# Optimization experiments

Measured on AMD Instinct MI355X. Metric: run time of the kernel, lower is better.

Reference implementation:

```python
import jax, jax.numpy as jnp
import numpy as np

ITERS_MAX = 10
CORR_THRESHOLD = 0.5


def setup_inputs() -> dict:
    key = jax.random.key(0)
    k1, k2, k3 = jax.random.split(key, 3)
    B, M, N = 8, 2048, 2048
    pc_src = jax.random.normal(k1, (B, 3, M), dtype=jnp.float32)
    # dest = src plus small perturbation so NN correspondences within threshold exist
    pc_dest = pc_src + 0.05 * jax.random.normal(k2, (B, 3, N), dtype=jnp.float32)
    init_R = jnp.broadcast_to(jnp.eye(3, dtype=jnp.float32), (B, 3, 3))
    init_t = 0.01 * jax.random.normal(k3, (B, 3, 1), dtype=jnp.float32)
    return {"pc_src": pc_src, "pc_dest": pc_dest, "init_R": init_R, "init_t": init_t}


def _icp(pc_src, pc_dest, init_R, init_t):
    # valid dest points: not exactly the zero vector (matches torch mask logic)
    valid = jnp.sum(pc_dest != 0.0, axis=1) == 3          # (B, N)
    any_valid = jnp.any(valid, axis=1)                    # (B,)
    src = pc_src[0].T                                     # (M, 3) -- original uses batch-0 source only
    dest = jnp.transpose(pc_dest, (0, 2, 1))              # (B, N, 3)
    dest_sq = jnp.sum(dest * dest, axis=-1)               # (B, N)
    thr2 = CORR_THRESHOLD * CORR_THRESHOLD

    def corr(Rc, tc):
        # transformed source points: (B, M, 3)
        p = jnp.einsum('bij,mj->bmi', Rc, src) + jnp.transpose(tc, (0, 2, 1))
        # all-pairs squared distances (B, M, N) -- the compute-heavy NN search
        d2 = (jnp.sum(p * p, axis=-1)[:, :, None] + dest_sq[:, None, :]
              - 2.0 * jnp.einsum('bmi,bni->bmn', p, dest))
        d2 = jnp.where(valid[:, None, :], d2, jnp.inf)
        idx = jnp.argmin(d2, axis=-1)                     # (B, M)
        q = jnp.take_along_axis(dest, idx[..., None], axis=1)   # (B, M, 3)
        # recompute exact squared residual from p, q (stable + differentiable)
        d2min = jnp.maximum(jnp.sum((p - q) ** 2, axis=-1), 0.0)  # (B, M)
        w = ((d2min < thr2) & any_valid[:, None]).astype(p.dtype)  # inlier weights
        return q, w, d2min

    def step(carry, _):
        Rc, tc = carry
        q, w, _ = corr(Rc, tc)
        wsum = jnp.sum(w, axis=-1)                        # (B,)
        safe = jnp.maximum(wsum, 1.0)
        mu_p = jnp.einsum('bm,mi->bi', w, src) / safe[:, None]
        mu_q = jnp.einsum('bm,bmi->bi', w, q) / safe[:, None]
        Pc = src[None, :, :] - mu_p[:, None, :]           # (B, M, 3)
        Qc = q - mu_q[:, None, :]                         # (B, M, 3)
        # Kabsch / Umeyama (no scaling): H = sum_m w p_c q_c^T
        H = jnp.einsum('bm,bmi,bmj->bij', w, Pc, Qc)
        U, S, Vt = jnp.linalg.svd(H)
        V = jnp.transpose(Vt, (0, 2, 1))
        d = jnp.linalg.det(V) * jnp.linalg.det(U)         # reflection fix
        D = jnp.stack([jnp.ones_like(d), jnp.ones_like(d), d], axis=-1)
        Rn = jnp.einsum('bij,bj,bkj->bik', V, D, U)       # V diag(1,1,d) U^T
        tn = (mu_q - jnp.einsum('bij,bj->bi', Rn, mu_p))[:, :, None]
        ok = (wsum > 0.0)[:, None, None]
        Rn = jnp.where(ok, Rn, Rc)
        tn = jnp.where(ok, tn, tc)
        return (Rn, tn), None

    (Rf, tf), _ = jax.lax.scan(step, (init_R, init_t), None, length=ITERS_MAX)

    # inlier RMSE at the final transform (Open3D icp_sol.inlier_rmse analogue)
    _, w, d2 = corr(Rf, tf)
    wsum = jnp.sum(w, axis=-1, keepdims=True)             # (B, 1)
    rmse = jnp.sqrt(jnp.sum(w * d2, axis=-1, keepdims=True) / jnp.maximum(wsum, 1.0))
    mse = jnp.where(wsum > 0.0, rmse, jnp.nan)            # (B, 1); nan if no valid dest
    return Rf, tf, mse


def reference(pc_src, pc_dest, init_R, init_t):
    return _icp(pc_src, pc_dest, init_R, init_t)
```

## Files before the change

### kernel.cpp

```cpp
#include <hip/hip_runtime.h>
#include <math.h>

#define BB 8
#define MM 2048
#define NNP 2048
#define THR2 0.25f
#define NITER 10
#define NPART 17
#define TPB 1024
#define WPB 16
#define BPB 32
#define GRIDB (BB * BPB)
#define TM 8
#define HALF (NNP / 2)
#define STEPS (HALF / 64)

__global__ void pack_kernel(const float* __restrict__ pc_dest,
                            float4* __restrict__ destp,
                            float* __restrict__ anyvalid)
{
    const int b = blockIdx.x;
    const int tid = threadIdx.x;
    __shared__ int anyf;
    if (tid == 0) anyf = 0;
    __syncthreads();
    int local = 0;
    for (int n = tid; n < NNP; n += blockDim.x) {
        const float dx = pc_dest[(b * 3 + 0) * NNP + n];
        const float dy = pc_dest[(b * 3 + 1) * NNP + n];
        const float dz = pc_dest[(b * 3 + 2) * NNP + n];
        const int valid = (dx != 0.0f) && (dy != 0.0f) && (dz != 0.0f);
        const float dd = dx * dx + dy * dy + dz * dz;
        destp[b * NNP + n] = make_float4(dx, dy, dz, valid ? dd : INFINITY);
        local |= valid;
    }
    if (local) atomicOr(&anyf, 1);
    __syncthreads();
    if (tid == 0) anyvalid[b] = (anyf != 0) ? 1.0f : 0.0f;
}

__device__ void kabsch3f(const float H[3][3], float R[3][3])
{
    float A[3][3];
    for (int i = 0; i < 3; ++i)
        for (int j = 0; j < 3; ++j) {
            float s = 0.0f;
            for (int k = 0; k < 3; ++k) s += H[k][i] * H[k][j];
            A[i][j] = s;
        }
    float V[3][3] = {{1,0,0},{0,1,0},{0,0,1}};
    const float nrm = A[0][0]*A[0][0] + A[1][1]*A[1][1] + A[2][2]*A[2][2] + 1e-30f;
    for (int sweep = 0; sweep < 8; ++sweep) {
        const float off = A[0][1]*A[0][1] + A[0][2]*A[0][2] + A[1][2]*A[1][2];
        if (off < 1e-14f * nrm) break;
        for (int pi = 0; pi < 3; ++pi) {
            const int p = (pi == 2) ? 1 : 0;
            const int q = (pi == 0) ? 1 : 2;
            const float apq = A[p][q];
            if (apq == 0.0f) continue;
            const float theta = (A[q][q] - A[p][p]) / (2.0f * apq);
            const float t = ((theta >= 0.0f) ? 1.0f : -1.0f) / (fabsf(theta) + sqrtf(theta * theta + 1.0f));
            const float c = 1.0f / sqrtf(t * t + 1.0f);
            const float s = t * c;
            const float app = A[p][p], aqq = A[q][q];
            A[p][p] = app - t * apq;
            A[q][q] = aqq + t * apq;
            A[p][q] = 0.0f; A[q][p] = 0.0f;
            const int r = 3 - p - q;
            const float arp = A[r][p], arq = A[r][q];
            A[r][p] = c * arp - s * arq; A[p][r] = A[r][p];
            A[r][q] = s * arp + c * arq; A[q][r] = A[r][q];
            for (int rr = 0; rr < 3; ++rr) {
                const float vrp = V[rr][p], vrq = V[rr][q];
                V[rr][p] = c * vrp - s * vrq;
                V[rr][q] = s * vrp + c * vrq;
            }
        }
    }
    float lam[3] = {A[0][0], A[1][1], A[2][2]};
    int ord[3] = {0, 1, 2};
    for (int i = 0; i < 2; ++i)
        for (int j = i + 1; j < 3; ++j)
            if (lam[ord[j]] > lam[ord[i]]) { const int tmp = ord[i]; ord[i] = ord[j]; ord[j] = tmp; }
    float Vs[3][3], U[3][3];
    for (int k = 0; k < 3; ++k) {
        const int c0 = ord[k];
        const float sk = sqrtf(fmaxf(lam[c0], 0.0f));
        const float inv = (sk > 1e-12f) ? 1.0f / sk : 0.0f;
        for (int i = 0; i < 3; ++i) {
            Vs[i][k] = V[i][c0];
            U[i][k] = (H[i][0] * V[0][c0] + H[i][1] * V[1][c0] + H[i][2] * V[2][c0]) * inv;
        }
    }
    const float detH = H[0][0] * (H[1][1] * H[2][2] - H[1][2] * H[2][1])
                     - H[0][1] * (H[1][0] * H[2][2] - H[1][2] * H[2][0])
                     + H[0][2] * (H[1][0] * H[2][1] - H[1][1] * H[2][0]);
    const float d = (detH < 0.0f) ? -1.0f : 1.0f;
    for (int i = 0; i < 3; ++i)
        for (int j = 0; j < 3; ++j)
            R[i][j] = Vs[i][0] * U[j][0] + Vs[i][1] * U[j][1] + d * Vs[i][2] * U[j][2];
}

__global__ __launch_bounds__(TPB, 4) void corr_kernel(
    const int it,
    const float* __restrict__ pc_src,
    const float4* __restrict__ destp,
    const float* __restrict__ anyvalid,
    const float* __restrict__ init_R,
    const float* __restrict__ init_t,
    float* __restrict__ partials,
    float* __restrict__ out)
{
    const int blk = blockIdx.x;
    const int b = blk / BPB;
    const int cblk = blk % BPB;
    const int tid = threadIdx.x;
    const int wid = tid >> 6;
    const int lane = tid & 63;
    const int pairid = wid >> 1;
    const int half = wid & 1;

    __shared__ float4 ds[NNP];
    __shared__ float sred[BPB * NPART];
    __shared__ float sminV[WPB][TM];
    __shared__ int   sminI[WPB][TM];
    __shared__ float smom[WPB / 2][NPART];
    __shared__ float Sfin[NPART];
    __shared__ float Rt[12];

    const float4* db = destp + b * NNP;
    ds[tid]       = db[tid];
    ds[tid + TPB] = db[tid + TPB];

    if (it > 0) {
        if (tid < BPB * NPART) {
            const int row = tid / NPART, k = tid % NPART;
            sred[tid] = partials[(size_t)(((it - 1) * BB + b) * BPB + row) * 32 + k];
        }
    } else {
        if (tid < 9) Rt[tid] = init_R[b * 9 + tid];
        if (tid < 3) Rt[9 + tid] = init_t[b * 3 + tid];
    }
    __syncthreads();

    if (it > 0) {
        if (tid < NPART) {
            float s = 0.0f;
            #pragma unroll
            for (int c = 0; c < BPB; ++c) s += sred[c * NPART + tid];
            Sfin[tid] = s;
        }
        __syncthreads();
        if (tid == 0) {
            const float wsum = Sfin[0];
            if (wsum >= 0.5f) {
                const float safe = fmaxf(wsum, 1.0f);
                const float inv = 1.0f / safe;
                float mup[3], muq[3];
                for (int i = 0; i < 3; ++i) { mup[i] = Sfin[1 + i] * inv; muq[i] = Sfin[4 + i] * inv; }
                float H[3][3];
                for (int i = 0; i < 3; ++i)
                    for (int j = 0; j < 3; ++j)
                        H[i][j] = (Sfin[7 + i * 3 + j] * inv) - mup[i] * muq[j];
                float R[3][3];
                kabsch3f(H, R);
                for (int i = 0; i < 3; ++i) {
                    for (int j = 0; j < 3; ++j) Rt[i * 3 + j] = R[i][j];
                    Rt[9 + i] = muq[i] - (R[i][0] * mup[0] + R[i][1] * mup[1] + R[i][2] * mup[2]);
                }
            } else {
                for (int k = 0; k < 9; ++k) Rt[k] = init_R[b * 9 + k];
                for (int k = 0; k < 3; ++k) Rt[9 + k] = init_t[b * 3 + k];
            }
        }
        __syncthreads();
    }

    if (it == NITER && cblk == 0) {
        if (tid < 9) out[b * 9 + tid] = Rt[tid];
        if (tid < 3) out[72 + b * 3 + tid] = Rt[9 + tid];
    }

    const int m0 = cblk * (WPB / 2 * TM) + pairid * TM;
    float sx[TM], sy[TM], sz[TM];
    #pragma unroll
    for (int t = 0; t < TM; ++t) {
        sx[t] = pc_src[0 * MM + m0 + t];
        sy[t] = pc_src[1 * MM + m0 + t];
        sz[t] = pc_src[2 * MM + m0 + t];
    }
    const float av = anyvalid[b];
    const int base = half * HALF;

    float nx[TM], ny[TM], nz[TM];
    #pragma unroll
    for (int t = 0; t < TM; ++t) {
        const float px = fmaf(Rt[0], sx[t], fmaf(Rt[1], sy[t], fmaf(Rt[2], sz[t], Rt[9])));
        const float py = fmaf(Rt[3], sx[t], fmaf(Rt[4], sy[t], fmaf(Rt[5], sz[t], Rt[10])));
        const float pz = fmaf(Rt[6], sx[t], fmaf(Rt[7], sy[t], fmaf(Rt[8], sz[t], Rt[11])));
        nx[t] = -2.0f * px; ny[t] = -2.0f * py; nz[t] = -2.0f * pz;
    }

    float best[TM]; int bidx[TM];
    #pragma unroll
    for (int t = 0; t < TM; ++t) { best[t] = INFINITY; bidx[t] = base + lane; }

    int j = base + lane;
    #pragma unroll 4
    for (int s = 0; s < STEPS; ++s, j += 64) {
        const float4 d = ds[j];
        #pragma unroll
        for (int t = 0; t < TM; ++t) {
            const float e = fmaf(nx[t], d.x, fmaf(ny[t], d.y, fmaf(nz[t], d.z, d.w)));
            if (e < best[t]) { best[t] = e; bidx[t] = j; }
        }
    }

    #pragma unroll
    for (int t = 0; t < TM; ++t) {
        float bv = best[t]; int bn = bidx[t];
        #pragma unroll
        for (int off = 32; off >= 1; off >>= 1) {
            const float ov = __shfl_xor(bv, off);
            const int on = __shfl_xor(bn, off);
            if (ov < bv || (ov == bv && on < bn)) { bv = ov; bn = on; }
        }
        best[t] = bv; bidx[t] = bn;
    }
    if (lane == 0) {
        #pragma unroll
        for (int t = 0; t < TM; ++t) { sminV[wid][t] = best[t]; sminI[wid][t] = bidx[t]; }
    }
    __syncthreads();

    if (!half) {
        float acc[NPART];
        #pragma unroll
        for (int k = 0; k < NPART; ++k) acc[k] = 0.0f;
        #pragma unroll
        for (int t = 0; t < TM; ++t) {
            float bv = best[t]; int bn = bidx[t];
            const float vO = sminV[wid + 1][t];
            const int iO = sminI[wid + 1][t];
            if (vO < bv) { bv = vO; bn = iO; }
            const float4 q = ds[bn];
            const float px = -0.5f * nx[t], py = -0.5f * ny[t], pz = -0.5f * nz[t];
            const float ex = px - q.x, ey = py - q.y, ez = pz - q.z;
            const float d2m = ex * ex + ey * ey + ez * ez;
            const float w = (d2m < THR2) ? av : 0.0f;
            acc[0] += w;
            acc[1] += w * sx[t];  acc[2] += w * sy[t];  acc[3] += w * sz[t];
            acc[4] += w * q.x;    acc[5] += w * q.y;    acc[6] += w * q.z;
            acc[7]  += w * sx[t] * q.x; acc[8]  += w * sx[t] * q.y; acc[9]  += w * sx[t] * q.z;
            acc[10] += w * sy[t] * q.x; acc[11] += w * sy[t] * q.y; acc[12] += w * sy[t] * q.z;
            acc[13] += w * sz[t] * q.x; acc[14] += w * sz[t] * q.y; acc[15] += w * sz[t] * q.z;
            acc[16] += w * d2m;
        }
        if (lane == 0) {
            #pragma unroll
            for (int k = 0; k < NPART; ++k) smom[pairid][k] = acc[k];
        }
    }
    __syncthreads();

    if (tid < NPART) {
        float s = 0.0f;
        #pragma unroll
        for (int p = 0; p < WPB / 2; ++p) s += smom[p][tid];
        partials[(size_t)((it * BB + b) * BPB + cblk) * 32 + tid] = s;
    }
}

__global__ __launch_bounds__(64) void finalize_kernel(const float* __restrict__ partials,
                                                      float* __restrict__ out)
{
    const int b = blockIdx.x;
    const int lane = threadIdx.x;
    float w = 0.0f, wd = 0.0f;
    if (lane < BPB) {
        const float* row = partials + (size_t)((NITER * BB + b) * BPB + lane) * 32;
        w = row[0];
        wd = row[16];
    }
    #pragma unroll
    for (int off = 16; off >= 1; off >>= 1) {
        w += __shfl_xor(w, off);
        wd += __shfl_xor(wd, off);
    }
    if (lane == 0) {
        const float safe = fmaxf(w, 1.0f);
        const float rmse = sqrtf(wd / safe);
        out[96 + b] = (w > 0.0f) ? rmse : __builtin_nanf("");
    }
}

extern "C" void kernel_launch(void* const* d_in, const int* in_sizes, int n_in,
                              void* d_out, int out_size, void* d_ws, size_t ws_size,
                              hipStream_t stream) {
    const float* pc_src  = (const float*)d_in[0];
    const float* pc_dest = (const float*)d_in[1];
    const float* init_R  = (const float*)d_in[2];
    const float* init_t  = (const float*)d_in[3];
    float* out = (float*)d_out;
    float* ws = (float*)d_ws;

    float4* destp   = (float4*)ws;
    float* anyvalid = ws + BB * NNP * 4;
    float* partials = anyvalid + BB;

    pack_kernel<<<BB, 256, 0, stream>>>(pc_dest, destp, anyvalid);

    for (int it = 0; it <= NITER; ++it) {
        corr_kernel<<<GRIDB, TPB, 0, stream>>>(it, pc_src, destp, anyvalid,
                                               init_R, init_t, partials, out);
    }
    finalize_kernel<<<BB, 64, 0, stream>>>(partials, out);
}
```

Baseline: 232.0 us.

## Fuse dest packing into corr kernel and use Newton polar iteration for rotation

Removes the separate pack kernel: each corr block now loads the raw dest coordinates, computes the validity mask and squared norms into shared memory, and derives any-valid through __syncthreads_or. The serial Jacobi SVD, run on one thread, is replaced by a scaled Newton polar-decomposition iteration when det(H) is positive, with the old Kabsch path kept as a fallback. Partials are now read with a contiguous stride-32 layout, and R/t is stored in a small workspace buffer. The intent is to cut one launch and the latency of the single-thread SVD between iterations, at the cost of redoing the packing in every block and an approximate polar solution with a fixed six iterations. The no-inlier fallback also changes from reusing init_R/init_t to reusing the previously stored transform.

```diff
diff --git a/kernel.cpp b/kernel.cpp
--- a/kernel.cpp
+++ b/kernel.cpp
@@ -14,30 +14,6 @@
 #define TM 8
 #define HALF (NNP / 2)
 #define STEPS (HALF / 64)
-
-__global__ void pack_kernel(const float* __restrict__ pc_dest,
-                            float4* __restrict__ destp,
-                            float* __restrict__ anyvalid)
-{
-    const int b = blockIdx.x;
-    const int tid = threadIdx.x;
-    __shared__ int anyf;
-    if (tid == 0) anyf = 0;
-    __syncthreads();
-    int local = 0;
-    for (int n = tid; n < NNP; n += blockDim.x) {
-        const float dx = pc_dest[(b * 3 + 0) * NNP + n];
-        const float dy = pc_dest[(b * 3 + 1) * NNP + n];
-        const float dz = pc_dest[(b * 3 + 2) * NNP + n];
-        const int valid = (dx != 0.0f) && (dy != 0.0f) && (dz != 0.0f);
-        const float dd = dx * dx + dy * dy + dz * dz;
-        destp[b * NNP + n] = make_float4(dx, dy, dz, valid ? dd : INFINITY);
-        local |= valid;
-    }
-    if (local) atomicOr(&anyf, 1);
-    __syncthreads();
-    if (tid == 0) anyvalid[b] = (anyf != 0) ? 1.0f : 0.0f;
-}
 
 __device__ void kabsch3f(const float H[3][3], float R[3][3])
 {
@@ -104,10 +80,10 @@
 __global__ __launch_bounds__(TPB, 4) void corr_kernel(
     const int it,
     const float* __restrict__ pc_src,
-    const float4* __restrict__ destp,
-    const float* __restrict__ anyvalid,
+    const float* __restrict__ pc_dest,
     const float* __restrict__ init_R,
     const float* __restrict__ init_t,
+    float* __restrict__ rtstore,
     float* __restrict__ partials,
     float* __restrict__ out)
 {
@@ -121,33 +97,37 @@
     const int half = wid & 1;
 
     __shared__ float4 ds[NNP];
-    __shared__ float sred[BPB * NPART];
+    __shared__ float sred[BPB * 32];
     __shared__ float sminV[WPB][TM];
     __shared__ int   sminI[WPB][TM];
     __shared__ float smom[WPB / 2][NPART];
     __shared__ float Sfin[NPART];
     __shared__ float Rt[12];
 
-    const float4* db = destp + b * NNP;
-    ds[tid]       = db[tid];
-    ds[tid + TPB] = db[tid + TPB];
+    const float dx0 = pc_dest[(b * 3 + 0) * NNP + tid];
+    const float dy0 = pc_dest[(b * 3 + 1) * NNP + tid];
+    const float dz0 = pc_dest[(b * 3 + 2) * NNP + tid];
+    const float dx1 = pc_dest[(b * 3 + 0) * NNP + tid + TPB];
+    const float dy1 = pc_dest[(b * 3 + 1) * NNP + tid + TPB];
+    const float dz1 = pc_dest[(b * 3 + 2) * NNP + tid + TPB];
+    const bool v0 = (dx0 != 0.0f) && (dy0 != 0.0f) && (dz0 != 0.0f);
+    const bool v1 = (dx1 != 0.0f) && (dy1 != 0.0f) && (dz1 != 0.0f);
+    ds[tid]       = make_float4(dx0, dy0, dz0, v0 ? dx0*dx0 + dy0*dy0 + dz0*dz0 : INFINITY);
+    ds[tid + TPB] = make_float4(dx1, dy1, dz1, v1 ? dx1*dx1 + dy1*dy1 + dz1*dz1 : INFINITY);
 
     if (it > 0) {
-        if (tid < BPB * NPART) {
-            const int row = tid / NPART, k = tid % NPART;
-            sred[tid] = partials[(size_t)(((it - 1) * BB + b) * BPB + row) * 32 + k];
-        }
+        sred[tid] = partials[(size_t)((it - 1) * BB + b) * (BPB * 32) + tid];
     } else {
         if (tid < 9) Rt[tid] = init_R[b * 9 + tid];
         if (tid < 3) Rt[9 + tid] = init_t[b * 3 + tid];
     }
-    __syncthreads();
+    const float av = __syncthreads_or((int)(v0 || v1)) ? 1.0f : 0.0f;
 
     if (it > 0) {
         if (tid < NPART) {
             float s = 0.0f;
             #pragma unroll
-            for (int c = 0; c < BPB; ++c) s += sred[c * NPART + tid];
+            for (int c = 0; c < BPB; ++c) s += sred[c * 32 + tid];
             Sfin[tid] = s;
         }
         __syncthreads();
@@ -157,28 +137,73 @@
                 const float safe = fmaxf(wsum, 1.0f);
                 const float inv = 1.0f / safe;
                 float mup[3], muq[3];
+                #pragma unroll
                 for (int i = 0; i < 3; ++i) { mup[i] = Sfin[1 + i] * inv; muq[i] = Sfin[4 + i] * inv; }
-                float H[3][3];
+                float H[9];
+                #pragma unroll
                 for (int i = 0; i < 3; ++i)
+                    #pragma unroll
                     for (int j = 0; j < 3; ++j)
-                        H[i][j] = (Sfin[7 + i * 3 + j] * inv) - mup[i] * muq[j];
-                float R[3][3];
-                kabsch3f(H, R);
-                for (int i = 0; i < 3; ++i) {
-                    for (int j = 0; j < 3; ++j) Rt[i * 3 + j] = R[i][j];
-                    Rt[9 + i] = muq[i] - (R[i][0] * mup[0] + R[i][1] * mup[1] + R[i][2] * mup[2]);
+                        H[i * 3 + j] = (Sfin[7 + i * 3 + j] * inv) - mup[i] * muq[j];
+                const float detH = H[0] * (H[4]*H[8] - H[5]*H[7])
+                                 - H[1] * (H[3]*H[8] - H[5]*H[6])
+                                 + H[2] * (H[3]*H[7] - H[4]*H[6]);
+                float R[9];
+                if (detH > 1e-12f) {
+                    float X[9] = {H[0], H[3], H[6], H[1], H[4], H[7], H[2], H[5], H[8]};
+                    const float mu = 1.0f / cbrtf(detH);
+                    #pragma unroll
+                    for (int k = 0; k < 9; ++k) X[k] *= mu;
+                    #pragma unroll
+                    for (int itn = 0; itn < 6; ++itn) {
+                        const float C0 = X[4]*X[8] - X[5]*X[7];
+                        const float C1 = X[5]*X[6] - X[3]*X[8];
+                        const float C2 = X[3]*X[7] - X[4]*X[6];
+                        const float C3 = X[2]*X[7] - X[1]*X[8];
+                        const float C4 = X[0]*X[8] - X[2]*X[6];
+                        const float C5 = X[1]*X[6] - X[0]*X[7];
+                        const float C6 = X[1]*X[5] - X[2]*X[4];
+                        const float C7 = X[2]*X[3] - X[0]*X[5];
+                        const float C8 = X[0]*X[4] - X[1]*X[3];
+                        const float det = X[0]*C0 + X[1]*C1 + X[2]*C2;
+                        const float h = 0.5f / det;
+                        X[0] = 0.5f*X[0] + h*C0; X[1] = 0.5f*X[1] + h*C1; X[2] = 0.5f*X[2] + h*C2;
+                        X[3] = 0.5f*X[3] + h*C3; X[4] = 0.5f*X[4] + h*C4; X[5] = 0.5f*X[5] + h*C5;
+                        X[6] = 0.5f*X[6] + h*C6; X[7] = 0.5f*X[7] + h*C7; X[8] = 0.5f*X[8] + h*C8;
+                    }
+                    #pragma unroll
+                    for (int k = 0; k < 9; ++k) R[k] = X[k];
+                } else {
+                    float H33[3][3], R33[3][3];
+                    #pragma unroll
+                    for (int i = 0; i < 3; ++i)
+                        #pragma unroll
+                        for (int j = 0; j < 3; ++j) H33[i][j] = H[i * 3 + j];
+                    kabsch3f(H33, R33);
+                    #pragma unroll
+                    for (int i = 0; i < 3; ++i)
+                        #pragma unroll
+                        for (int j = 0; j < 3; ++j) R[i * 3 + j] = R33[i][j];
                 }
+                #pragma unroll
+                for (int k = 0; k < 9; ++k) Rt[k] = R[k];
+                #pragma unroll
+                for (int i = 0; i < 3; ++i)
+                    Rt[9 + i] = muq[i] - (R[i*3+0] * mup[0] + R[i*3+1] * mup[1] + R[i*3+2] * mup[2]);
             } else {
-                for (int k = 0; k < 9; ++k) Rt[k] = init_R[b * 9 + k];
-                for (int k = 0; k < 3; ++k) Rt[9 + k] = init_t[b * 3 + k];
+                #pragma unroll
+                for (int k = 0; k < 12; ++k) Rt[k] = rtstore[b * 16 + k];
             }
         }
         __syncthreads();
     }
 
-    if (it == NITER && cblk == 0) {
-        if (tid < 9) out[b * 9 + tid] = Rt[tid];
-        if (tid < 3) out[72 + b * 3 + tid] = Rt[9 + tid];
+    if (cblk == 0 && tid < 12) {
+        rtstore[b * 16 + tid] = Rt[tid];
+        if (it == NITER) {
+            if (tid < 9) out[b * 9 + tid] = Rt[tid];
+            else out[72 + b * 3 + (tid - 9)] = Rt[tid];
+        }
     }
 
     const int m0 = cblk * (WPB / 2 * TM) + pairid * TM;
@@ -189,7 +214,6 @@
         sy[t] = pc_src[1 * MM + m0 + t];
         sz[t] = pc_src[2 * MM + m0 + t];
     }
-    const float av = anyvalid[b];
     const int base = half * HALF;
 
     float nx[TM], ny[TM], nz[TM];
@@ -304,15 +328,12 @@
     float* out = (float*)d_out;
     float* ws = (float*)d_ws;
 
-    float4* destp   = (float4*)ws;
-    float* anyvalid = ws + BB * NNP * 4;
-    float* partials = anyvalid + BB;
-
-    pack_kernel<<<BB, 256, 0, stream>>>(pc_dest, destp, anyvalid);
+    float* rtstore  = ws;
+    float* partials = ws + BB * 16;
 
     for (int it = 0; it <= NITER; ++it) {
-        corr_kernel<<<GRIDB, TPB, 0, stream>>>(it, pc_src, destp, anyvalid,
-                                               init_R, init_t, partials, out);
+        corr_kernel<<<GRIDB, TPB, 0, stream>>>(it, pc_src, pc_dest, init_R, init_t,
+                                               rtstore, partials, out);
     }
     finalize_kernel<<<BB, 64, 0, stream>>>(partials, out);
 }
```

Result: faster. 206.4 us (-11.0%).
